# Performance work log

Measured on AMD Instinct MI355X. Metric: run time of the kernel, lower is better.

## Reference

```python
import jax, jax.numpy as jnp
import numpy as np

N, E, VD, HD, ES = 10000, 80000, 32, 64, 68
NET_IN = VD * VD + 2 * HD + ES   # 1220: f2s(1024) + s[e0](64) + s[e1](64) + edge_s(68)
SELF_IN = VD * VD + 2 * HD       # 1152: temp_f2s(1024) + s(64) + s_c(64)
OUT_D = VD * VD + HD             # 1088: vector channel mixer + scalar update


def _lecun(k, fin, fout):
    return jax.random.normal(k, (fin, fout), jnp.float32) / jnp.sqrt(jnp.float32(fin))


def setup_inputs() -> dict:
    ks = jax.random.split(jax.random.key(0), 16)
    return {
        "f": jax.random.normal(ks[0], (N, 3, VD), jnp.float32),
        "s": jax.random.normal(ks[1], (N, HD), jnp.float32),
        "edge_f": jax.random.normal(ks[2], (E, 3, 1), jnp.float32),
        "edge_s": jax.random.normal(ks[3], (E, ES), jnp.float32),
        "W_emb1": _lecun(ks[4], 2 * VD + 1, VD),
        "net_W1": _lecun(ks[5], NET_IN, HD), "net_b1": jnp.zeros((HD,), jnp.float32),
        "net_W2": _lecun(ks[6], HD, HD), "net_b2": jnp.zeros((HD,), jnp.float32),
        "net_W3": _lecun(ks[7], HD, OUT_D), "net_b3": jnp.zeros((OUT_D,), jnp.float32),
        "W_emb2": _lecun(ks[8], 2 * VD, VD),
        "self_W1": _lecun(ks[9], SELF_IN, HD), "self_b1": jnp.zeros((HD,), jnp.float32),
        "self_W2": _lecun(ks[10], HD, HD), "self_b2": jnp.zeros((HD,), jnp.float32),
        "self_W3": _lecun(ks[11], HD, OUT_D), "self_b3": jnp.zeros((OUT_D,), jnp.float32),
        "edge_index": jax.random.randint(ks[12], (2, E), 0, N),
    }


def _mlp(x, W1, b1, W2, b2, W3, b3):
    h = jax.nn.relu(x @ W1 + b1)
    h = jax.nn.relu(h @ W2 + b2)
    return h @ W3 + b3


def _segment_mean(x, ids, n):
    tot = jax.ops.segment_sum(x, ids, num_segments=n)
    cnt = jax.ops.segment_sum(jnp.ones(ids.shape, x.dtype), ids, num_segments=n)
    return tot / jnp.maximum(cnt, 1.0).reshape((n,) + (1,) * (x.ndim - 1))


def _forward(f, s, edge_f, edge_s,
             W_emb1, net_W1, net_b1, net_W2, net_b2, net_W3, net_b3,
             W_emb2, self_W1, self_b1, self_W2, self_b2, self_W3, self_b3,
             edge_index):
    n = f.shape[0]
    e0, e1 = edge_index[0], edge_index[1]
    # --- edge message: gather -> embed -> gram einsum -> MLP ---
    _f = jnp.concatenate((f[e0], f[e1], edge_f), axis=-1)          # [E,3,2VD+1]
    _s = jnp.concatenate((s[e0], s[e1], edge_s), axis=-1)          # [E,2HD+ES]
    _f = _f @ W_emb1                                               # [E,3,VD]
    f2s = jnp.einsum('eij,eik->ejk', _f, _f).reshape(-1, VD * VD)  # _f^T @ _f, [E,VD*VD]
    Fn = jnp.linalg.norm(f2s, axis=-1, keepdims=True) + 1.0
    c = _mlp(jnp.concatenate((f2s, _s), axis=-1),
             net_W1, net_b1, net_W2, net_b2, net_W3, net_b3) / Fn  # [E,OUT_D]
    f_c = jnp.einsum('eij,ejk->eik', _f, c[:, :VD * VD].reshape(-1, VD, VD))  # [E,3,VD]
    f_c = _segment_mean(f_c, e0, n)                                # [N,3,VD]
    s_c = _segment_mean(c[:, VD * VD:], e0, n)                     # [N,HD]
    # --- node self-update ---
    tf = jnp.concatenate((f, f_c), axis=-1) @ W_emb2               # [N,3,VD]
    tf2s = jnp.einsum('nij,nik->njk', tf, tf).reshape(n, VD * VD)
    Fn2 = jnp.linalg.norm(tf2s, axis=-1, keepdims=True) + 1.0
    c2 = _mlp(jnp.concatenate((tf2s, s, s_c), axis=-1),
              self_W1, self_b1, self_W2, self_b2, self_W3, self_b3) / Fn2
    f_out = jnp.einsum('nij,njk->nik', tf, c2[:, :VD * VD].reshape(-1, VD, VD)) + f
    s_out = c2[:, VD * VD:] + s
    return f_out, s_out


def reference(f, s, edge_f, edge_s,
              W_emb1, net_W1, net_b1, net_W2, net_b2, net_W3, net_b3,
              W_emb2, self_W1, self_b1, self_W2, self_b2, self_W3, self_b3,
              edge_index):
    return _forward(f, s, edge_f, edge_s,
                    W_emb1, net_W1, net_b1, net_W2, net_b2, net_W3, net_b3,
                    W_emb2, self_W1, self_b1, self_W2, self_b2, self_W3, self_b3,
                    edge_index)
```

## Files before the change

kernel.cpp:

```cpp
#include <hip/hip_runtime.h>
#include <math.h>

#define NN 10000
#define NE 80000
#define SF 97
#define STX 72
#define NTRI 528
#define SAE 104
#define SAN 72

typedef __attribute__((ext_vector_type(8))) __bf16 bf16x8;
typedef __attribute__((ext_vector_type(8))) short short8v;
typedef __attribute__((ext_vector_type(4))) float f32x4;
typedef __attribute__((ext_vector_type(4))) unsigned uint4v;

__device__ __forceinline__ ushort f2bf(float x) {
  union { float f; unsigned u; } v; v.f = x;
  unsigned r = v.u + 0x7FFFu + ((v.u >> 16) & 1u);
  return (ushort)(r >> 16);
}
__device__ __forceinline__ float bf2f(ushort u) {
  union { unsigned u; float f; } v; v.u = (unsigned)u << 16;
  return v.f;
}
__device__ __forceinline__ void tri_ab(int k, int& a, int& b) {
  int aa = 0, rem = k;
  while (rem >= 32 - aa) { rem -= 32 - aa; ++aa; }
  a = aa; b = aa + rem;
}

__global__ __launch_bounds__(256)
void sgnn_hist(const int* __restrict__ eidx, int* __restrict__ deg) {
  const int e = blockIdx.x * 256 + threadIdx.x;
  if (e < NE) atomicAdd(deg + eidx[e], 1);
}

__global__ __launch_bounds__(1024)
void sgnn_scan(const int* __restrict__ deg, int* __restrict__ cursor,
               int* __restrict__ start) {
  __shared__ int sm[1024];
  __shared__ int carry;
  const int t = threadIdx.x;
  if (t == 0) carry = 0;
  __syncthreads();
  for (int base = 0; base < NN; base += 1024) {
    const int i = base + t;
    const int v = (i < NN) ? deg[i] : 0;
    sm[t] = v;
    __syncthreads();
    #pragma unroll
    for (int d = 1; d < 1024; d <<= 1) {
      const int add = (t >= d) ? sm[t - d] : 0;
      __syncthreads();
      sm[t] += add;
      __syncthreads();
    }
    const int excl = carry + sm[t] - v;
    if (i < NN) { cursor[i] = excl; start[i] = excl; }
    __syncthreads();
    if (t == 1023) carry += sm[1023];
    __syncthreads();
  }
}

__global__ __launch_bounds__(256)
void sgnn_scatter(const int* __restrict__ eidx, int* __restrict__ cursor,
                  int* __restrict__ sorted) {
  const int e = blockIdx.x * 256 + threadIdx.x;
  if (e < NE) {
    const int p = atomicAdd(cursor + eidx[e], 1);
    sorted[p] = e;
  }
}

__global__ __launch_bounds__(256)
void sgnn_wconv(const float* __restrict__ nW1, const float* __restrict__ nW2,
                const float* __restrict__ nW3, const float* __restrict__ sW1,
                const float* __restrict__ sW2, const float* __restrict__ sW3,
                const float* __restrict__ Wemb1, const float* __restrict__ Wemb2,
                ushort* __restrict__ wout, ushort* __restrict__ tab) {
  const int gid = blockIdx.x * 256 + threadIdx.x;
  if (gid >= 61 * 4096) {
    const int k = gid - 61 * 4096;
    if (k < NTRI) {
      int a, b; tri_ab(k, a, b);
      tab[k] = (ushort)(a | (b << 8) | ((a != b) ? 0x8000 : 0));
    }
    return;
  }
  const int tile = gid >> 12, idx = gid & 4095;
  const int c = idx >> 6, k = idx & 63;
  float v = 0.f;
  if (tile < 12) {
    const int T = tile;
    if (T < 8 || (T == 8 && k < 16)) {
      const int ktri = T * 64 + k;
      if (ktri < NTRI) {
        int a, b; tri_ab(ktri, a, b);
        v = nW1[(a * 32 + b) * 64 + c];
        if (a != b) v += nW1[(b * 32 + a) * 64 + c];
      }
    } else if (T == 8) { if (k < 20) v = nW1[(1216 + (k - 16)) * 64 + c]; }
    else if (T == 9)   v = nW1[(1024 + k) * 64 + c];
    else if (T == 10)  v = nW1[(1088 + k) * 64 + c];
    else               v = nW1[(1152 + k) * 64 + c];
  } else if (tile == 12) v = nW2[k * 64 + c];
  else if (tile < 30)    v = nW3[k * 1088 + (tile - 13) * 64 + c];
  else if (tile < 41) {
    const int T = tile - 30;
    if (T < 8 || (T == 8 && k < 16)) {
      const int ktri = T * 64 + k;
      if (ktri < NTRI) {
        int a, b; tri_ab(ktri, a, b);
        v = sW1[(a * 32 + b) * 64 + c];
        if (a != b) v += sW1[(b * 32 + a) * 64 + c];
      }
    } else if (T == 9) v = sW1[(1024 + k) * 64 + c];
    else if (T == 10)  v = sW1[(1088 + k) * 64 + c];
  } else if (tile == 41) v = sW2[k * 64 + c];
  else if (tile < 59)    v = sW3[k * 1088 + (tile - 42) * 64 + c];
  else if (tile == 59) {
    const int col = idx / 96, kk = idx % 96;
    v = (col < 32 && kk < 65) ? Wemb1[kk * 32 + col] : 0.f;
  } else {
    const int col = idx >> 6;
    v = (col < 32) ? Wemb2[k * 32 + col] : 0.f;
  }
  wout[gid] = f2bf(v);
}

#define STAGE_W(srcbase) do { const ushort* _s = (srcbase);                      \
  _Pragma("unroll") for (int rr = 0; rr < 2; ++rr) {                             \
    const int idx_ = t + 256 * rr; const int c_ = idx_ >> 3, ko_ = idx_ & 7;     \
    *(short8v*)&Wl[c_ * STX + ko_ * 8] = *(const short8v*)&_s[c_ * 64 + ko_ * 8];\
  } } while (0)

#define WPRE_LOAD(srcbase) do { const ushort* _s = (srcbase);                    \
  wpre0 = *(const short8v*)&_s[(t >> 3) * 64 + (t & 7) * 8];                     \
  wpre1 = *(const short8v*)&_s[(32 + (t >> 3)) * 64 + (t & 7) * 8]; } while (0)

#define WPRE_STORE() do {                                                        \
  *(short8v*)&Wl[(t >> 3) * STX + (t & 7) * 8] = wpre0;                          \
  *(short8v*)&Wl[(32 + (t >> 3)) * STX + (t & 7) * 8] = wpre1; } while (0)

#define MFMA_K64() do {                                                          \
  _Pragma("unroll") for (int kb = 0; kb < 2; ++kb) {                             \
    const bf16x8 af_ = *(const bf16x8*)&Xl[(w * 16 + ll) * STX + kb * 32 + lh * 8]; \
    acc[0] = __builtin_amdgcn_mfma_f32_16x16x32_bf16(af_,                        \
        *(const bf16x8*)&Wl[(     ll) * STX + kb * 32 + lh * 8], acc[0], 0, 0, 0); \
    acc[1] = __builtin_amdgcn_mfma_f32_16x16x32_bf16(af_,                        \
        *(const bf16x8*)&Wl[(16 + ll) * STX + kb * 32 + lh * 8], acc[1], 0, 0, 0); \
    acc[2] = __builtin_amdgcn_mfma_f32_16x16x32_bf16(af_,                        \
        *(const bf16x8*)&Wl[(32 + ll) * STX + kb * 32 + lh * 8], acc[2], 0, 0, 0); \
    acc[3] = __builtin_amdgcn_mfma_f32_16x16x32_bf16(af_,                        \
        *(const bf16x8*)&Wl[(48 + ll) * STX + kb * 32 + lh * 8], acc[3], 0, 0, 0); \
  } } while (0)

#define ZERO_ACC() do { _Pragma("unroll") for (int q = 0; q < 4; ++q)            \
    acc[q] = (f32x4){0.f, 0.f, 0.f, 0.f}; } while (0)

#define PACK_STORE16(dstp) do {                                                  \
  unsigned pk[8];                                                                \
  _Pragma("unroll") for (int q = 0; q < 8; ++q)                                  \
    pk[q] = (unsigned)f2bf(xv[2 * q]) | ((unsigned)f2bf(xv[2 * q + 1]) << 16);   \
  *(uint4v*)(dstp)       = (uint4v){pk[0], pk[1], pk[2], pk[3]};                 \
  *(uint4v*)((dstp) + 8) = (uint4v){pk[4], pk[5], pk[6], pk[7]};                 \
} while (0)

#define TRI16(kt) do {                                                           \
  int prev_a = -1; float fa0 = 0.f, fa1 = 0.f, fa2 = 0.f;                        \
  _Pragma("unroll") for (int m = 0; m < 16; ++m) {                               \
    const int tb = tabL[(kt) + m];                                               \
    const int a_ = tb & 31, b_ = (tb >> 8) & 31;                                 \
    if (a_ != prev_a) { fa0 = fr[a_]; fa1 = fr[32 + a_]; fa2 = fr[64 + a_];      \
                        prev_a = a_; }                                           \
    const float v = fmaf(fa0, fr[b_],                                            \
        fmaf(fa1, fr[32 + b_], fa2 * fr[64 + b_]));                              \
    const float wsel = (tb & 0x8000) ? 2.f : 1.f;                                \
    sumsq = fmaf(v * wsel, v, sumsq);                                            \
    xv[m] = v;                                                                   \
  } } while (0)

#define XV_LOAD16(p) do { const float* _p = (p);                                 \
  _Pragma("unroll") for (int q = 0; q < 4; ++q) {                                \
    const float4 v4 = *(const float4*)(_p + 4 * q);                              \
    xv[4 * q + 0] = v4.x; xv[4 * q + 1] = v4.y;                                  \
    xv[4 * q + 2] = v4.z; xv[4 * q + 3] = v4.w; } } while (0)

#define LDS_BYTES 53152

__global__ __launch_bounds__(256, 2)
void sgnn_edge(const float* __restrict__ f, const float* __restrict__ s,
               const float* __restrict__ edge_f, const float* __restrict__ edge_s,
               const float* __restrict__ b1, const float* __restrict__ b2,
               const float* __restrict__ b3,
               const ushort* __restrict__ wbf, const ushort* __restrict__ tab_g,
               const int* __restrict__ eidx, const int* __restrict__ sorted,
               const int* __restrict__ start_g, const int* __restrict__ deg_g,
               float* __restrict__ fc_sum, float* __restrict__ sc_sum) {
  __shared__ __align__(16) char sbuf[LDS_BYTES];
  float*  smF  = (float*)sbuf;
  ushort* Xl   = (ushort*)(sbuf + 24832);
  ushort* Wl   = (ushort*)(sbuf + 34048);
  ushort* Aemb = (ushort*)(sbuf + 24832);
  float*  red  = (float*)(sbuf + 43264);
  ushort* C2h  = (ushort*)(sbuf + 43264);
  ushort* tabL = (ushort*)(sbuf + 51584);
  float*  iFn  = (float*)(sbuf + 51584);
  int*    es_s = (int*)(sbuf + 52640);
  ushort* e0s  = (ushort*)(sbuf + 52896);
  ushort* e1s  = (ushort*)(sbuf + 53024);
  float*  fcpart = (float*)(sbuf + 24832);
  float*  scpart = (float*)(sbuf + 24832 + 3072);
  int*    snode  = (int*)(sbuf + 24832 + 5120);
  int*    sst    = (int*)(sbuf + 24832 + 5152);
  int*    sdg    = (int*)(sbuf + 24832 + 5184);

  const int t = threadIdx.x, j = t & 63, w = t >> 6, eb = w * 16;
  const int lh = j >> 4, ll = j & 15;
  const int bid = blockIdx.x;
  const ushort* wembT = wbf + 59 * 4096;
  short8v wpre0, wpre1;

  if (t < 64) {
    const int e = sorted[bid * 64 + t];
    es_s[t] = e;
    e0s[t] = (ushort)eidx[e];
    e1s[t] = (ushort)eidx[NE + e];
  }
  for (int idx = t; idx < NTRI; idx += 256) tabL[idx] = tab_g[idx];
  __syncthreads();

  int str = 0, dgr = 0;
  if (j < 16) {
    const int n_ = e0s[eb + j];
    str = start_g[n_];
    dgr = deg_g[n_];
  }
  WPRE_LOAD(wbf + 0);

  #pragma unroll 1
  for (int h = 0; h < 2; ++h) {
    const int hb = h * 32;
    #pragma unroll 1
    for (int cc = t; cc < 576; cc += 256) {
      const int row = cc / 6, seg = cc - row * 6;
      const int lel = (row * 43) >> 7, il = row - lel * 3;
      const int k0 = seg * 16;
      float xv[16];
      if (seg < 4) {
        const int nd = (seg < 2) ? (int)e0s[hb + lel] : (int)e1s[hb + lel];
        XV_LOAD16(f + nd * 96 + il * 32 + (seg & 1) * 16);
      } else if (seg == 4) {
        xv[0] = edge_f[es_s[hb + lel] * 3 + il];
        #pragma unroll
        for (int m = 1; m < 16; ++m) xv[m] = 0.f;
      } else {
        #pragma unroll
        for (int m = 0; m < 16; ++m) xv[m] = 0.f;
      }
      PACK_STORE16(&Aemb[row * SAE + k0]);
    }
    __syncthreads();
    #pragma unroll 1
    for (int job = w * 3; job < w * 3 + 3; ++job) {
      const int mt = job >> 1, nt = job & 1;
      f32x4 ac = (f32x4){0.f, 0.f, 0.f, 0.f};
      #pragma unroll
      for (int kb = 0; kb < 3; ++kb) {
        const bf16x8 av = *(const bf16x8*)&Aemb[(mt * 16 + ll) * SAE + kb * 32 + lh * 8];
        const bf16x8 bv = *(const bf16x8*)&wembT[(nt * 16 + ll) * 96 + kb * 32 + lh * 8];
        ac = __builtin_amdgcn_mfma_f32_16x16x32_bf16(av, bv, ac, 0, 0, 0);
      }
      #pragma unroll
      for (int r = 0; r < 4; ++r) {
        const int rr = mt * 16 + lh * 4 + r;
        const int lel = (rr * 43) >> 7, il = rr - lel * 3;
        smF[(hb + lel) * SF + il * 32 + nt * 16 + ll] = ac[r];
      }
    }
    __syncthreads();
  }

  f32x4 acc[4];
  ZERO_ACC();
  float sumsq = 0.f;

  #pragma unroll 1
  for (int T = 0; T < 12; ++T) {
    __syncthreads();
    WPRE_STORE();
    {
      const float* fr = smF + j * SF;
      float xv[16];
      if (T < 8) {
        TRI16(T * 64 + w * 16);
      } else if (T == 8) {
        if (w == 0) {
          TRI16(512);
        } else if (w == 1) {
          const float4 v4 = *(const float4*)(edge_s + es_s[j] * 68 + 64);
          xv[0] = v4.x; xv[1] = v4.y; xv[2] = v4.z; xv[3] = v4.w;
          #pragma unroll
          for (int m = 4; m < 16; ++m) xv[m] = 0.f;
        } else {
          #pragma unroll
          for (int m = 0; m < 16; ++m) xv[m] = 0.f;
        }
      } else if (T == 9)  { XV_LOAD16(s + e0s[j] * 64 + w * 16); }
      else if (T == 10)   { XV_LOAD16(s + e1s[j] * 64 + w * 16); }
      else                { XV_LOAD16(edge_s + es_s[j] * 68 + w * 16); }
      PACK_STORE16(&Xl[j * STX + w * 16]);
    }
    __syncthreads();
    WPRE_LOAD(wbf + (T + 1) * 4096);
    MFMA_K64();
  }

  __syncthreads();
  red[w * 64 + j] = sumsq;
  #pragma unroll
  for (int nc = 0; nc < 4; ++nc) {
    const float bv = b1[nc * 16 + ll];
    #pragma unroll
    for (int r = 0; r < 4; ++r)
      Xl[(w * 16 + lh * 4 + r) * STX + nc * 16 + ll] = f2bf(fmaxf(acc[nc][r] + bv, 0.f));
  }
  WPRE_STORE();
  ZERO_ACC();
  __syncthreads();
  if (t < 64) {
    const float ss = red[t] + red[64 + t] + red[128 + t] + red[192 + t];
    iFn[t] = 1.f / (sqrtf(ss) + 1.f);
  }

  MFMA_K64();
  #pragma unroll
  for (int nc = 0; nc < 4; ++nc) {
    const float bv = b2[nc * 16 + ll];
    #pragma unroll
    for (int r = 0; r < 4; ++r)
      Xl[(w * 16 + lh * 4 + r) * STX + nc * 16 + ll] = f2bf(fmaxf(acc[nc][r] + bv, 0.f));
  }

  float fcp[48];
  #pragma unroll
  for (int q = 0; q < 48; ++q) fcp[q] = 0.f;
  float csv[16];

  #pragma unroll 1
  for (int nt = 0; nt < 17; ++nt) {
    __syncthreads();
    STAGE_W(wbf + (13 + nt) * 4096);
    __syncthreads();
    ZERO_ACC();
    MFMA_K64();
    #pragma unroll
    for (int nc = 0; nc < 4; ++nc)
      #pragma unroll
      for (int r = 0; r < 4; ++r)
        C2h[(w * 16 + lh * 4 + r) * 65 + nc * 16 + ll] = f2bf(acc[nc][r]);
    const float bv = b3[nt * 64 + j];
    if (nt < 16) {
      const int a_ = nt * 2 + (j >> 5);
      #pragma unroll
      for (int m = 0; m < 16; ++m) {
        const float cv = (bf2f(C2h[(eb + m) * 65 + j]) + bv) * iFn[eb + m];
        const float* fr = smF + (eb + m) * SF;
        fcp[m * 3 + 0] = fmaf(fr[a_],      cv, fcp[m * 3 + 0]);
        fcp[m * 3 + 1] = fmaf(fr[32 + a_], cv, fcp[m * 3 + 1]);
        fcp[m * 3 + 2] = fmaf(fr[64 + a_], cv, fcp[m * 3 + 2]);
      }
    } else {
      #pragma unroll
      for (int m = 0; m < 16; ++m)
        csv[m] = (bf2f(C2h[(eb + m) * 65 + j]) + bv) * iFn[eb + m];
    }
  }

  __syncthreads();
  if (t < 8) snode[t] = -1;
  __syncthreads();

  {
    float r0 = 0.f, r1 = 0.f, r2 = 0.f, rs = 0.f;
    int runlen = 0;
    const int gwb = bid * 64 + eb;
    #pragma unroll
    for (int m = 0; m < 16; ++m) {
      float v0 = fcp[m * 3 + 0]; v0 += __shfl_xor(v0, 32);
      float v1 = fcp[m * 3 + 1]; v1 += __shfl_xor(v1, 32);
      float v2 = fcp[m * 3 + 2]; v2 += __shfl_xor(v2, 32);
      r0 += v0; r1 += v1; r2 += v2; rs += csv[m];
      ++runlen;
      const int n = e0s[eb + m];
      if (m == 15 || e0s[eb + m + 1] != n) {
        const int st = __shfl(str, m);
        const int dg = __shfl(dgr, m);
        const int g1v = gwb + m, g0v = g1v - runlen + 1;
        if (g0v == st && runlen == dg) {
          if (j < 32) {
            fc_sum[n * 96 + j]      = r0;
            fc_sum[n * 96 + 32 + j] = r1;
            fc_sum[n * 96 + 64 + j] = r2;
          }
          sc_sum[n * 64 + j] = rs;
        } else {
          const int slot = (g0v == gwb) ? 2 * w : 2 * w + 1;
          if (j < 32) {
            fcpart[slot * 96 + j]      = r0;
            fcpart[slot * 96 + 32 + j] = r1;
            fcpart[slot * 96 + 64 + j] = r2;
          }
          scpart[slot * 64 + j] = rs;
          if (j == 0) { snode[slot] = n; sst[slot] = st; sdg[slot] = dg; }
        }
        r0 = r1 = r2 = rs = 0.f; runlen = 0;
      }
    }
  }
  __syncthreads();

  if (t < 160) {
    const int ch = t;
    int prevn = -1;
    #pragma unroll 1
    for (int ss = 0; ss < 8; ++ss) {
      const int n = snode[ss];
      if (n < 0) { continue; }
      if (n != prevn) {
        float v = (ch < 96) ? fcpart[ss * 96 + ch] : scpart[ss * 64 + (ch - 96)];
        #pragma unroll 1
        for (int k2 = ss + 1; k2 < 8; ++k2) {
          if (snode[k2] == n)
            v += (ch < 96) ? fcpart[k2 * 96 + ch] : scpart[k2 * 64 + (ch - 96)];
          else if (snode[k2] >= 0) break;
        }
        const bool cib = (sst[ss] >= bid * 64) && (sst[ss] + sdg[ss] <= bid * 64 + 64);
        float* dst = (ch < 96) ? (fc_sum + n * 96 + ch) : (sc_sum + n * 64 + (ch - 96));
        if (cib) *dst = v; else atomicAdd(dst, v);
      }
      prevn = n;
    }
  }
}

__global__ __launch_bounds__(256)
void sgnn_norm(float* __restrict__ fcm, float* __restrict__ scm,
               const int* __restrict__ deg) {
  const int idx = blockIdx.x * 256 + threadIdx.x;
  if (idx >= NN * 160) return;
  const int n = idx / 160, c = idx % 160;
  const float ic = 1.f / fmaxf((float)deg[n], 1.f);
  if (c < 96) fcm[n * 96 + c] *= ic;
  else        scm[n * 64 + (c - 96)] *= ic;
}

__global__ __launch_bounds__(256, 2)
void sgnn_node(const float* __restrict__ f, const float* __restrict__ s,
               const float* __restrict__ b1, const float* __restrict__ b2,
               const float* __restrict__ b3,
               const ushort* __restrict__ wbf, const ushort* __restrict__ tab_g,
               const float* __restrict__ fcm, const float* __restrict__ scm,
               float* __restrict__ of, float* __restrict__ os) {
  __shared__ __align__(16) char sbuf[LDS_BYTES];
  float*  smF  = (float*)sbuf;
  ushort* Xl   = (ushort*)(sbuf + 24832);
  ushort* Wl   = (ushort*)(sbuf + 34048);
  ushort* Aemb = (ushort*)(sbuf + 24832);
  float*  red  = (float*)(sbuf + 43264);
  ushort* C2h  = (ushort*)(sbuf + 43264);
  ushort* tabL = (ushort*)(sbuf + 51584);
  float*  iFn  = (float*)(sbuf + 51584);

  const int t = threadIdx.x, j = t & 63, w = t >> 6, eb = w * 16;
  const int lh = j >> 4, ll = j & 15;
  const int nbase = blockIdx.x * 64;
  const ushort* wembTn = wbf + 60 * 4096;
  short8v wpre0, wpre1;

  for (int idx = t; idx < NTRI; idx += 256) tabL[idx] = tab_g[idx];
  WPRE_LOAD(wbf + 30 * 4096);
  __syncthreads();

  #pragma unroll 1
  for (int h = 0; h < 2; ++h) {
    const int hb = h * 32;
    #pragma unroll 1
    for (int cc = t; cc < 384; cc += 256) {
      const int row = cc >> 2, seg = cc & 3;
      const int lel = (row * 43) >> 7, il = row - lel * 3;
      const int nc = min(nbase + hb + lel, NN - 1);
      const int k0 = seg * 16;
      float xv[16];
      const float* p = (seg < 2) ? (f + nc * 96 + il * 32 + seg * 16)
                                 : (fcm + nc * 96 + il * 32 + (seg - 2) * 16);
      XV_LOAD16(p);
      PACK_STORE16(&Aemb[row * SAN + k0]);
    }
    __syncthreads();
    #pragma unroll 1
    for (int job = w * 3; job < w * 3 + 3; ++job) {
      const int mt = job >> 1, nt = job & 1;
      f32x4 ac = (f32x4){0.f, 0.f, 0.f, 0.f};
      #pragma unroll
      for (int kb = 0; kb < 2; ++kb) {
        const bf16x8 av = *(const bf16x8*)&Aemb[(mt * 16 + ll) * SAN + kb * 32 + lh * 8];
        const bf16x8 bv = *(const bf16x8*)&wembTn[(nt * 16 + ll) * 64 + kb * 32 + lh * 8];
        ac = __builtin_amdgcn_mfma_f32_16x16x32_bf16(av, bv, ac, 0, 0, 0);
      }
      #pragma unroll
      for (int r = 0; r < 4; ++r) {
        const int rr = mt * 16 + lh * 4 + r;
        const int lel = (rr * 43) >> 7, il = rr - lel * 3;
        smF[(hb + lel) * SF + il * 32 + nt * 16 + ll] = ac[r];
      }
    }
    __syncthreads();
  }

  f32x4 acc[4];
  ZERO_ACC();
  float sumsq = 0.f;

  #pragma unroll 1
  for (int T = 0; T < 11; ++T) {
    __syncthreads();
    WPRE_STORE();
    {
      const float* fr = smF + j * SF;
      float xv[16];
      if (T < 8) {
        TRI16(T * 64 + w * 16);
      } else if (T == 8) {
        if (w == 0) {
          TRI16(512);
        } else {
          #pragma unroll
          for (int m = 0; m < 16; ++m) xv[m] = 0.f;
        }
      } else if (T == 9) {
        XV_LOAD16(s + min(nbase + j, NN - 1) * 64 + w * 16);
      } else {
        XV_LOAD16(scm + min(nbase + j, NN - 1) * 64 + w * 16);
      }
      PACK_STORE16(&Xl[j * STX + w * 16]);
    }
    __syncthreads();
    WPRE_LOAD(wbf + (31 + T) * 4096);
    MFMA_K64();
  }

  __syncthreads();
  red[w * 64 + j] = sumsq;
  #pragma unroll
  for (int nc = 0; nc < 4; ++nc) {
    const float bv = b1[nc * 16 + ll];
    #pragma unroll
    for (int r = 0; r < 4; ++r)
      Xl[(w * 16 + lh * 4 + r) * STX + nc * 16 + ll] = f2bf(fmaxf(acc[nc][r] + bv, 0.f));
  }
  WPRE_STORE();
  ZERO_ACC();
  __syncthreads();
  if (t < 64) {
    const float ss = red[t] + red[64 + t] + red[128 + t] + red[192 + t];
    iFn[t] = 1.f / (sqrtf(ss) + 1.f);
  }

  MFMA_K64();
  #pragma unroll
  for (int nc = 0; nc < 4; ++nc) {
    const float bv = b2[nc * 16 + ll];
    #pragma unroll
    for (int r = 0; r < 4; ++r)
      Xl[(w * 16 + lh * 4 + r) * STX + nc * 16 + ll] = f2bf(fmaxf(acc[nc][r] + bv, 0.f));
  }

  float fcp[48];
  #pragma unroll
  for (int q = 0; q < 48; ++q) fcp[q] = 0.f;

  #pragma unroll 1
  for (int nt = 0; nt < 17; ++nt) {
    __syncthreads();
    STAGE_W(wbf + (42 + nt) * 4096);
    __syncthreads();
    ZERO_ACC();
    MFMA_K64();
    #pragma unroll
    for (int nc = 0; nc < 4; ++nc)
      #pragma unroll
      for (int r = 0; r < 4; ++r)
        C2h[(w * 16 + lh * 4 + r) * 65 + nc * 16 + ll] = f2bf(acc[nc][r]);
    const float bv = b3[nt * 64 + j];
    if (nt < 16) {
      const int a_ = nt * 2 + (j >> 5);
      #pragma unroll
      for (int m = 0; m < 16; ++m) {
        const float cv = (bf2f(C2h[(eb + m) * 65 + j]) + bv) * iFn[eb + m];
        const float* fr = smF + (eb + m) * SF;
        fcp[m * 3 + 0] = fmaf(fr[a_],      cv, fcp[m * 3 + 0]);
        fcp[m * 3 + 1] = fmaf(fr[32 + a_], cv, fcp[m * 3 + 1]);
        fcp[m * 3 + 2] = fmaf(fr[64 + a_], cv, fcp[m * 3 + 2]);
      }
    } else {
      #pragma unroll
      for (int m = 0; m < 16; ++m) {
        const int n_m = nbase + eb + m;
        const float cv = (bf2f(C2h[(eb + m) * 65 + j]) + bv) * iFn[eb + m];
        if (n_m < NN) os[n_m * 64 + j] = cv + s[n_m * 64 + j];
      }
    }
  }

  {
    const int b_ = j & 31;
    #pragma unroll
    for (int m = 0; m < 16; ++m) {
      const int n_m = nbase + eb + m;
      #pragma unroll
      for (int i = 0; i < 3; ++i) {
        float v = fcp[m * 3 + i];
        v += __shfl_xor(v, 32);
        if (j < 32 && n_m < NN)
          of[n_m * 96 + i * 32 + b_] = v + f[n_m * 96 + i * 32 + b_];
      }
    }
  }
}

extern "C" void kernel_launch(void* const* d_in, const int* in_sizes, int n_in,
                              void* d_out, int out_size, void* d_ws, size_t ws_size,
                              hipStream_t stream) {
  const float* f      = (const float*)d_in[0];
  const float* s      = (const float*)d_in[1];
  const float* edge_f = (const float*)d_in[2];
  const float* edge_s = (const float*)d_in[3];
  const float* Wemb1  = (const float*)d_in[4];
  const float* nW1 = (const float*)d_in[5];
  const float* nb1 = (const float*)d_in[6];
  const float* nW2 = (const float*)d_in[7];
  const float* nb2 = (const float*)d_in[8];
  const float* nW3 = (const float*)d_in[9];
  const float* nb3 = (const float*)d_in[10];
  const float* Wemb2 = (const float*)d_in[11];
  const float* sW1 = (const float*)d_in[12];
  const float* sb1 = (const float*)d_in[13];
  const float* sW2 = (const float*)d_in[14];
  const float* sb2 = (const float*)d_in[15];
  const float* sW3 = (const float*)d_in[16];
  const float* sb3 = (const float*)d_in[17];
  const int* eidx  = (const int*)d_in[18];

  float* of = (float*)d_out;
  float* os = of + (size_t)NN * 96;

  int* deg    = (int*)d_ws;
  int* cursor = deg + NN;
  int* start  = cursor + NN;
  int* sorted = start + NN;
  ushort* wbf = (ushort*)(sorted + NE);
  ushort* tab = wbf + 61 * 4096;

  hipMemsetAsync(deg, 0, (size_t)NN * 4, stream);
  hipMemsetAsync(d_out, 0, (size_t)NN * 160 * 4, stream);

  hipLaunchKernelGGL(sgnn_wconv, dim3((61 * 4096 + NTRI + 255) / 256), dim3(256),
                     0, stream, nW1, nW2, nW3, sW1, sW2, sW3, Wemb1, Wemb2,
                     wbf, tab);
  hipLaunchKernelGGL(sgnn_hist, dim3((NE + 255) / 256), dim3(256), 0, stream,
                     eidx, deg);
  hipLaunchKernelGGL(sgnn_scan, dim3(1), dim3(1024), 0, stream, deg, cursor, start);
  hipLaunchKernelGGL(sgnn_scatter, dim3((NE + 255) / 256), dim3(256), 0, stream,
                     eidx, cursor, sorted);
  hipLaunchKernelGGL(sgnn_edge, dim3(NE / 64), dim3(256), 0, stream,
                     f, s, edge_f, edge_s, nb1, nb2, nb3,
                     wbf, tab, eidx, sorted, start, deg,
                     of , os );
  hipLaunchKernelGGL(sgnn_norm, dim3((NN * 160 + 255) / 256), dim3(256), 0, stream,
                     of, os, deg);
  hipLaunchKernelGGL(sgnn_node, dim3((NN + 63) / 64), dim3(256), 0, stream,
                     f, s, sb1, sb2, sb3,
                     wbf, tab, of , os , of, os);
}
```

Before: 238.5 us.

## Consume MFMA outputs from registers, fold mean normalization into node kernel

The final MLP layer's accumulators are now used directly from registers in both the edge and node kernels. Before, they were written to LDS as bf16 and read back per row. The per-edge vector contraction is restructured around the MFMA output layout, and results are staged once into LDS for the segment reduction and output writes. The separate normalization kernel is removed, and the node kernel scales fc/sc by the inverse degree as it loads them. This saves a bf16 round-trip, LDS traffic and one launch, in exchange for a more complex reduction path and changed LDS layouts.

```diff
diff --git a/kernel.cpp b/kernel.cpp
--- a/kernel.cpp
+++ b/kernel.cpp
@@ -3,7 +3,8 @@
 
 #define NN 10000
 #define NE 80000
-#define SF 97
+#define SF 98
+#define SFF 97
 #define STX 72
 #define NTRI 528
 #define SAE 104
@@ -18,10 +19,6 @@
   union { float f; unsigned u; } v; v.f = x;
   unsigned r = v.u + 0x7FFFu + ((v.u >> 16) & 1u);
   return (ushort)(r >> 16);
-}
-__device__ __forceinline__ float bf2f(ushort u) {
-  union { unsigned u; float f; } v; v.u = (unsigned)u << 16;
-  return v.f;
 }
 __device__ __forceinline__ void tri_ab(int k, int& a, int& b) {
   int aa = 0, rem = k;
@@ -187,7 +184,36 @@
     xv[4 * q + 0] = v4.x; xv[4 * q + 1] = v4.y;                                  \
     xv[4 * q + 2] = v4.z; xv[4 * q + 3] = v4.w; } } while (0)
 
-#define LDS_BYTES 53152
+#define CONSUME_NT() do {                                                        \
+  _Pragma("unroll") for (int r = 0; r < 4; ++r) {                                \
+    const int row_ = w * 16 + lh * 4 + r;                                        \
+    float2 fr2_0 = *(const float2*)&smF[row_ * SF +      nt * 2];                \
+    float2 fr2_1 = *(const float2*)&smF[row_ * SF + 32 + nt * 2];                \
+    float2 fr2_2 = *(const float2*)&smF[row_ * SF + 64 + nt * 2];                \
+    _Pragma("unroll") for (int nc = 0; nc < 4; ++nc) {                           \
+      const float cv = (acc[nc][r] + b3v[nc]) * ifnr[r];                         \
+      const int p = nc & 1;                                                      \
+      const float f0 = (nc < 2) ? fr2_0.x : fr2_0.y;                             \
+      const float f1 = (nc < 2) ? fr2_1.x : fr2_1.y;                             \
+      const float f2 = (nc < 2) ? fr2_2.x : fr2_2.y;                             \
+      fch[(r * 3 + 0) * 2 + p] = fmaf(f0, cv, fch[(r * 3 + 0) * 2 + p]);         \
+      fch[(r * 3 + 1) * 2 + p] = fmaf(f1, cv, fch[(r * 3 + 1) * 2 + p]);         \
+      fch[(r * 3 + 2) * 2 + p] = fmaf(f2, cv, fch[(r * 3 + 2) * 2 + p]);         \
+    }                                                                            \
+  } } while (0)
+
+#define STAGE_FS() do {                                                          \
+  _Pragma("unroll") for (int r = 0; r < 4; ++r) {                                \
+    const int row_ = w * 16 + lh * 4 + r;                                        \
+    _Pragma("unroll") for (int i = 0; i < 3; ++i) {                              \
+      F[row_ * SFF + i * 32 + ll]      = fch[(r * 3 + i) * 2 + 0];               \
+      F[row_ * SFF + i * 32 + ll + 16] = fch[(r * 3 + i) * 2 + 1];               \
+    }                                                                            \
+    _Pragma("unroll") for (int nc = 0; nc < 4; ++nc)                             \
+      S[row_ * 65 + nc * 16 + ll] = cs[nc * 4 + r];                              \
+  } } while (0)
+
+#define LDS_BYTES 46624
 
 __global__ __launch_bounds__(256, 2)
 void sgnn_edge(const float* __restrict__ f, const float* __restrict__ s,
@@ -200,21 +226,22 @@
                float* __restrict__ fc_sum, float* __restrict__ sc_sum) {
   __shared__ __align__(16) char sbuf[LDS_BYTES];
   float*  smF  = (float*)sbuf;
-  ushort* Xl   = (ushort*)(sbuf + 24832);
-  ushort* Wl   = (ushort*)(sbuf + 34048);
-  ushort* Aemb = (ushort*)(sbuf + 24832);
-  float*  red  = (float*)(sbuf + 43264);
-  ushort* C2h  = (ushort*)(sbuf + 43264);
-  ushort* tabL = (ushort*)(sbuf + 51584);
-  float*  iFn  = (float*)(sbuf + 51584);
-  int*    es_s = (int*)(sbuf + 52640);
-  ushort* e0s  = (ushort*)(sbuf + 52896);
-  ushort* e1s  = (ushort*)(sbuf + 53024);
-  float*  fcpart = (float*)(sbuf + 24832);
-  float*  scpart = (float*)(sbuf + 24832 + 3072);
-  int*    snode  = (int*)(sbuf + 24832 + 5120);
-  int*    sst    = (int*)(sbuf + 24832 + 5152);
-  int*    sdg    = (int*)(sbuf + 24832 + 5184);
+  float*  F    = (float*)sbuf;
+  ushort* Xl   = (ushort*)(sbuf + 25088);
+  ushort* Wl   = (ushort*)(sbuf + 34304);
+  ushort* Aemb = (ushort*)(sbuf + 25088);
+  float*  S    = (float*)(sbuf + 25088);
+  float*  red  = (float*)(sbuf + 43520);
+  int*    snode = (int*)(sbuf + 43520);
+  int*    srow0 = snode + 8;
+  int*    srow1 = snode + 16;
+  int*    sst   = snode + 24;
+  int*    sdg   = snode + 32;
+  ushort* tabL = (ushort*)(sbuf + 45056);
+  float*  iFn  = (float*)(sbuf + 45056);
+  int*    es_s = (int*)(sbuf + 46112);
+  ushort* e0s  = (ushort*)(sbuf + 46368);
+  ushort* e1s  = (ushort*)(sbuf + 46496);
 
   const int t = threadIdx.x, j = t & 63, w = t >> 6, eb = w * 16;
   const int lh = j >> 4, ll = j & 15;
@@ -343,79 +370,70 @@
       Xl[(w * 16 + lh * 4 + r) * STX + nc * 16 + ll] = f2bf(fmaxf(acc[nc][r] + bv, 0.f));
   }
 
-  float fcp[48];
+  float fch[24];
   #pragma unroll
-  for (int q = 0; q < 48; ++q) fcp[q] = 0.f;
-  float csv[16];
+  for (int q = 0; q < 24; ++q) fch[q] = 0.f;
+  float cs[16];
+  float ifnr[4];
 
   #pragma unroll 1
   for (int nt = 0; nt < 17; ++nt) {
     __syncthreads();
     STAGE_W(wbf + (13 + nt) * 4096);
-    __syncthreads();
+    float b3v[4];
+    #pragma unroll
+    for (int nc = 0; nc < 4; ++nc) b3v[nc] = b3[nt * 64 + nc * 16 + ll];
+    __syncthreads();
+    if (nt == 0) {
+      #pragma unroll
+      for (int r = 0; r < 4; ++r) ifnr[r] = iFn[w * 16 + lh * 4 + r];
+    }
     ZERO_ACC();
     MFMA_K64();
-    #pragma unroll
-    for (int nc = 0; nc < 4; ++nc)
-      #pragma unroll
-      for (int r = 0; r < 4; ++r)
-        C2h[(w * 16 + lh * 4 + r) * 65 + nc * 16 + ll] = f2bf(acc[nc][r]);
-    const float bv = b3[nt * 64 + j];
     if (nt < 16) {
-      const int a_ = nt * 2 + (j >> 5);
-      #pragma unroll
-      for (int m = 0; m < 16; ++m) {
-        const float cv = (bf2f(C2h[(eb + m) * 65 + j]) + bv) * iFn[eb + m];
-        const float* fr = smF + (eb + m) * SF;
-        fcp[m * 3 + 0] = fmaf(fr[a_],      cv, fcp[m * 3 + 0]);
-        fcp[m * 3 + 1] = fmaf(fr[32 + a_], cv, fcp[m * 3 + 1]);
-        fcp[m * 3 + 2] = fmaf(fr[64 + a_], cv, fcp[m * 3 + 2]);
-      }
+      CONSUME_NT();
     } else {
       #pragma unroll
-      for (int m = 0; m < 16; ++m)
-        csv[m] = (bf2f(C2h[(eb + m) * 65 + j]) + bv) * iFn[eb + m];
-    }
-  }
-
-  __syncthreads();
+      for (int nc = 0; nc < 4; ++nc)
+        #pragma unroll
+        for (int r = 0; r < 4; ++r)
+          cs[nc * 4 + r] = (acc[nc][r] + b3v[nc]) * ifnr[r];
+    }
+  }
+
+  __syncthreads();
+  STAGE_FS();
   if (t < 8) snode[t] = -1;
   __syncthreads();
 
   {
-    float r0 = 0.f, r1 = 0.f, r2 = 0.f, rs = 0.f;
+    float r0 = 0.f, r1 = 0.f, rs = 0.f;
     int runlen = 0;
     const int gwb = bid * 64 + eb;
-    #pragma unroll
+    #pragma unroll 1
     for (int m = 0; m < 16; ++m) {
-      float v0 = fcp[m * 3 + 0]; v0 += __shfl_xor(v0, 32);
-      float v1 = fcp[m * 3 + 1]; v1 += __shfl_xor(v1, 32);
-      float v2 = fcp[m * 3 + 2]; v2 += __shfl_xor(v2, 32);
-      r0 += v0; r1 += v1; r2 += v2; rs += csv[m];
+      const int row = eb + m;
+      r0 += F[row * SFF + j];
+      if (j < 32) r1 += F[row * SFF + 64 + j];
+      rs += S[row * 65 + j];
       ++runlen;
-      const int n = e0s[eb + m];
-      if (m == 15 || e0s[eb + m + 1] != n) {
+      const int n = e0s[row];
+      if (m == 15 || e0s[row + 1] != n) {
         const int st = __shfl(str, m);
         const int dg = __shfl(dgr, m);
         const int g1v = gwb + m, g0v = g1v - runlen + 1;
         if (g0v == st && runlen == dg) {
-          if (j < 32) {
-            fc_sum[n * 96 + j]      = r0;
-            fc_sum[n * 96 + 32 + j] = r1;
-            fc_sum[n * 96 + 64 + j] = r2;
-          }
+          fc_sum[n * 96 + j] = r0;
+          if (j < 32) fc_sum[n * 96 + 64 + j] = r1;
           sc_sum[n * 64 + j] = rs;
         } else {
           const int slot = (g0v == gwb) ? 2 * w : 2 * w + 1;
-          if (j < 32) {
-            fcpart[slot * 96 + j]      = r0;
-            fcpart[slot * 96 + 32 + j] = r1;
-            fcpart[slot * 96 + 64 + j] = r2;
+          if (j == 0) {
+            snode[slot] = n; srow0[slot] = row - runlen + 1; srow1[slot] = row;
+            sst[slot] = st; sdg[slot] = dg;
           }
-          scpart[slot * 64 + j] = rs;
-          if (j == 0) { snode[slot] = n; sst[slot] = st; sdg[slot] = dg; }
         }
-        r0 = r1 = r2 = rs = 0.f; runlen = 0;
+        r0 = r1 = rs = 0.f; runlen = 0;
       }
     }
   }
@@ -427,14 +445,16 @@
     #pragma unroll 1
     for (int ss = 0; ss < 8; ++ss) {
       const int n = snode[ss];
-      if (n < 0) { continue; }
+      if (n < 0) continue;
       if (n != prevn) {
-        float v = (ch < 96) ? fcpart[ss * 96 + ch] : scpart[ss * 64 + (ch - 96)];
+        float v = 0.f;
         #pragma unroll 1
-        for (int k2 = ss + 1; k2 < 8; ++k2) {
-          if (snode[k2] == n)
-            v += (ch < 96) ? fcpart[k2 * 96 + ch] : scpart[k2 * 64 + (ch - 96)];
-          else if (snode[k2] >= 0) break;
+        for (int k2 = ss; k2 < 8; ++k2) {
+          if (snode[k2] == n) {
+            #pragma unroll 1
+            for (int row = srow0[k2]; row <= srow1[k2]; ++row)
+              v += (ch < 96) ? F[row * SFF + ch] : S[row * 65 + (ch - 96)];
+          } else if (k2 > ss && snode[k2] >= 0) break;
         }
         const bool cib = (sst[ss] >= bid * 64) && (sst[ss] + sdg[ss] <= bid * 64 + 64);
         float* dst = (ch < 96) ? (fc_sum + n * 96 + ch) : (sc_sum + n * 64 + (ch - 96));
@@ -443,17 +463,6 @@
       prevn = n;
     }
   }
-}
-
-__global__ __launch_bounds__(256)
-void sgnn_norm(float* __restrict__ fcm, float* __restrict__ scm,
-               const int* __restrict__ deg) {
-  const int idx = blockIdx.x * 256 + threadIdx.x;
-  if (idx >= NN * 160) return;
-  const int n = idx / 160, c = idx % 160;
-  const float ic = 1.f / fmaxf((float)deg[n], 1.f);
-  if (c < 96) fcm[n * 96 + c] *= ic;
-  else        scm[n * 64 + (c - 96)] *= ic;
 }
 
 __global__ __launch_bounds__(256, 2)
@@ -462,16 +471,19 @@
                const float* __restrict__ b3,
                const ushort* __restrict__ wbf, const ushort* __restrict__ tab_g,
                const float* __restrict__ fcm, const float* __restrict__ scm,
+               const int* __restrict__ deg_g,
                float* __restrict__ of, float* __restrict__ os) {
   __shared__ __align__(16) char sbuf[LDS_BYTES];
   float*  smF  = (float*)sbuf;
-  ushort* Xl   = (ushort*)(sbuf + 24832);
-  ushort* Wl   = (ushort*)(sbuf + 34048);
-  ushort* Aemb = (ushort*)(sbuf + 24832);
-  float*  red  = (float*)(sbuf + 43264);
-  ushort* C2h  = (ushort*)(sbuf + 43264);
-  ushort* tabL = (ushort*)(sbuf + 51584);
-  float*  iFn  = (float*)(sbuf + 51584);
+  float*  F    = (float*)sbuf;
+  ushort* Xl   = (ushort*)(sbuf + 25088);
+  ushort* Wl   = (ushort*)(sbuf + 34304);
+  ushort* Aemb = (ushort*)(sbuf + 25088);
+  float*  S    = (float*)(sbuf + 25088);
+  float*  red  = (float*)(sbuf + 43520);
+  float*  icntL = (float*)(sbuf + 43520);
+  ushort* tabL = (ushort*)(sbuf + 45056);
+  float*  iFn  = (float*)(sbuf + 45056);
 
   const int t = threadIdx.x, j = t & 63, w = t >> 6, eb = w * 16;
   const int lh = j >> 4, ll = j & 15;
@@ -480,6 +492,8 @@
   short8v wpre0, wpre1;
 
   for (int idx = t; idx < NTRI; idx += 256) tabL[idx] = tab_g[idx];
+  if (t < 64)
+    icntL[t] = 1.f / fmaxf((float)deg_g[min(nbase + t, NN - 1)], 1.f);
   WPRE_LOAD(wbf + 30 * 4096);
   __syncthreads();
 
@@ -493,9 +507,14 @@
       const int nc = min(nbase + hb + lel, NN - 1);
       const int k0 = seg * 16;
       float xv[16];
-      const float* p = (seg < 2) ? (f + nc * 96 + il * 32 + seg * 16)
-                                 : (fcm + nc * 96 + il * 32 + (seg - 2) * 16);
-      XV_LOAD16(p);
+      if (seg < 2) {
+        XV_LOAD16(f + nc * 96 + il * 32 + seg * 16);
+      } else {
+        XV_LOAD16(fcm + nc * 96 + il * 32 + (seg - 2) * 16);
+        const float ic = icntL[hb + lel];
+        #pragma unroll
+        for (int m = 0; m < 16; ++m) xv[m] *= ic;
+      }
       PACK_STORE16(&Aemb[row * SAN + k0]);
     }
     __syncthreads();
@@ -543,6 +562,9 @@
         XV_LOAD16(s + min(nbase + j, NN - 1) * 64 + w * 16);
       } else {
         XV_LOAD16(scm + min(nbase + j, NN - 1) * 64 + w * 16);
+        const float ic = icntL[j];
+        #pragma unroll
+        for (int m = 0; m < 16; ++m) xv[m] *= ic;
       }
       PACK_STORE16(&Xl[j * STX + w * 16]);
     }
@@ -577,55 +599,50 @@
       Xl[(w * 16 + lh * 4 + r) * STX + nc * 16 + ll] = f2bf(fmaxf(acc[nc][r] + bv, 0.f));
   }
 
-  float fcp[48];
+  float fch[24];
   #pragma unroll
-  for (int q = 0; q < 48; ++q) fcp[q] = 0.f;
+  for (int q = 0; q < 24; ++q) fch[q] = 0.f;
+  float cs[16];
+  float ifnr[4];
 
   #pragma unroll 1
   for (int nt = 0; nt < 17; ++nt) {
     __syncthreads();
     STAGE_W(wbf + (42 + nt) * 4096);
-    __syncthreads();
+    float b3v[4];
+    #pragma unroll
+    for (int nc = 0; nc < 4; ++nc) b3v[nc] = b3[nt * 64 + nc * 16 + ll];
+    __syncthreads();
+    if (nt == 0) {
+      #pragma unroll
+      for (int r = 0; r < 4; ++r) ifnr[r] = iFn[w * 16 + lh * 4 + r];
+    }
     ZERO_ACC();
     MFMA_K64();
-    #pragma unroll
-    for (int nc = 0; nc < 4; ++nc)
-      #pragma unroll
-      for (int r = 0; r < 4; ++r)
-        C2h[(w * 16 + lh * 4 + r) * 65 + nc * 16 + ll] = f2bf(acc[nc][r]);
-    const float bv = b3[nt * 64 + j];
     if (nt < 16) {
-      const int a_ = nt * 2 + (j >> 5);
-      #pragma unroll
-      for (int m = 0; m < 16; ++m) {
-        const float cv = (bf2f(C2h[(eb + m) * 65 + j]) + bv) * iFn[eb + m];
-        const float* fr = smF + (eb + m) * SF;
-        fcp[m * 3 + 0] = fmaf(fr[a_],      cv, fcp[m * 3 + 0]);
-        fcp[m * 3 + 1] = fmaf(fr[32 + a_], cv, fcp[m * 3 + 1]);
-        fcp[m * 3 + 2] = fmaf(fr[64 + a_], cv, fcp[m * 3 + 2]);
-      }
+      CONSUME_NT();
     } else {
       #pragma unroll
-      for (int m = 0; m < 16; ++m) {
-        const int n_m = nbase + eb + m;
-        const float cv = (bf2f(C2h[(eb + m) * 65 + j]) + bv) * iFn[eb + m];
-        if (n_m < NN) os[n_m * 64 + j] = cv + s[n_m * 64 + j];
-      }
-    }
-  }
-
-  {
-    const int b_ = j & 31;
-    #pragma unroll
-    for (int m = 0; m < 16; ++m) {
-      const int n_m = nbase + eb + m;
-      #pragma unroll
-      for (int i = 0; i < 3; ++i) {
-        float v = fcp[m * 3 + i];
-        v += __shfl_xor(v, 32);
-        if (j < 32 && n_m < NN)
-          of[n_m * 96 + i * 32 + b_] = v + f[n_m * 96 + i * 32 + b_];
-      }
+      for (int nc = 0; nc < 4; ++nc)
+        #pragma unroll
+        for (int r = 0; r < 4; ++r)
+          cs[nc * 4 + r] = (acc[nc][r] + b3v[nc]) * ifnr[r];
+    }
+  }
+
+  __syncthreads();
+  STAGE_FS();
+  __syncthreads();
+
+  #pragma unroll 1
+  for (int m = 0; m < 16; ++m) {
+    const int row = eb + m;
+    const int n_m = nbase + row;
+    if (n_m < NN) {
+      of[n_m * 96 + j] = F[row * SFF + j] + f[n_m * 96 + j];
+      if (j < 32)
+        of[n_m * 96 + 64 + j] = F[row * SFF + 64 + j] + f[n_m * 96 + 64 + j];
+      os[n_m * 64 + j] = S[row * 65 + j] + s[n_m * 64 + j];
     }
   }
 }
@@ -678,9 +695,7 @@
                      f, s, edge_f, edge_s, nb1, nb2, nb3,
                      wbf, tab, eidx, sorted, start, deg,
                      of , os );
-  hipLaunchKernelGGL(sgnn_norm, dim3((NN * 160 + 255) / 256), dim3(256), 0, stream,
-                     of, os, deg);
   hipLaunchKernelGGL(sgnn_node, dim3((NN + 63) / 64), dim3(256), 0, stream,
                      f, s, sb1, sb2, sb3,
-                     wbf, tab, of , os , of, os);
-}
+                     wbf, tab, of , os , deg, of, os);
+}
```

Measured after the change: 210.8 us. -11.6%, faster.
